# Kernel optimization log

Hardware: AMD Instinct MI355X
Metric: run time of the kernel (lower is better)

## Reference

```python
import jax, jax.numpy as jnp
import numpy as np

N_RAYS = 262144
N_COARSE = 64
N_SAMPLES = 256
TFINAL = 1e10  # sentinel far plane for last integration delta
EPS = 1e-5


def setup_inputs() -> dict:
    key = jax.random.key(0)
    k1, k2, k3, k4, k5 = jax.random.split(key, 5)
    tnear = jax.random.uniform(k1, (N_RAYS, 1), jnp.float32) * 0.5 + 0.1
    tfar = tnear + 1.0 + jax.random.uniform(k2, (N_RAYS, 1), jnp.float32) * 3.0
    dnorm = jax.random.uniform(k3, (N_RAYS, 1), jnp.float32) * 0.5 + 0.75
    # density at the coarse sample points (stands in for vol.sample(rays(ts_coarse)))
    density = jax.random.uniform(k4, (N_COARSE, N_RAYS, 1), jnp.float32) * 5.0
    # uniform draws for inverse-CDF sampling (torch.rand in the original)
    u = jax.random.uniform(k5, (N_RAYS, N_SAMPLES), jnp.float32)
    return {"tnear": tnear, "tfar": tfar, "dnorm": dnorm, "density": density, "u": u}


def _informed_sampler(tnear, tfar, dnorm, density, u):
    Tc = density.shape[0]
    # --- batch_linspace: coarse ts, shape (Tc, N, 1), timestep dim leading ---
    frac = (jnp.arange(Tc, dtype=tnear.dtype) / (Tc - 1)).reshape(Tc, 1, 1)
    ts = tnear[None] + (tfar - tnear)[None] * frac
    # --- integrate_timesteps: volume-rendering weights, shape (Tc, N, 1) ---
    delta = jnp.concatenate(
        [ts[1:] - ts[:-1], jnp.full_like(ts[:1], TFINAL) - ts[-1:]], axis=0
    )
    sd = density * delta * dnorm[None]            # sigma * dt * |d|
    sd_shift = jnp.concatenate([jnp.zeros_like(sd[:1]), sd[:-1]], axis=0)
    transmittance = jnp.exp(-jnp.cumsum(sd_shift, axis=0))
    weights = transmittance * (1.0 - jnp.exp(-sd))
    # --- sample_ray_step_informed: CDF build + inverse-CDF resampling ---
    w = jnp.moveaxis(weights[..., 0], 0, -1) + EPS          # (N, Tc)
    pdf = w / jnp.sum(w, axis=-1, keepdims=True)
    cdf = jnp.concatenate(
        [jnp.zeros_like(pdf[..., :1]), jnp.cumsum(pdf, axis=-1)], axis=-1
    )                                                        # (N, Tc+1)
    tsn = jnp.moveaxis(ts[..., 0], 0, -1)                    # (N, Tc)
    # bin edges: [tnear, midpoints, tfar] -> (N, Tc+1), Tc bins match Tc weights
    edges = jnp.concatenate(
        [tnear, 0.5 * (tsn[..., 1:] + tsn[..., :-1]), tfar], axis=-1
    )
    # per-ray searchsorted (vmap avoids a (N, S, Tc+1) dense compare)
    idx = jax.vmap(lambda c, q: jnp.searchsorted(c, q, side="right"))(cdf, u)
    idx = jnp.clip(idx, 1, Tc)
    below = idx - 1
    cdf_b = jnp.take_along_axis(cdf, below, axis=-1)
    cdf_a = jnp.take_along_axis(cdf, idx, axis=-1)
    e_b = jnp.take_along_axis(edges, below, axis=-1)
    e_a = jnp.take_along_axis(edges, idx, axis=-1)
    denom = cdf_a - cdf_b
    denom = jnp.where(denom < EPS, jnp.ones_like(denom), denom)
    t = (u - cdf_b) / denom
    samples = jnp.sort(e_b + t * (e_a - e_b), axis=-1)       # (N, n_samples)
    return jnp.moveaxis(samples, -1, 0)[..., None]           # (n_samples, N, 1)


def reference(tnear, tfar, dnorm, density, u):
    return _informed_sampler(tnear, tfar, dnorm, density, u)
```

## Files before the change

kernel.cpp:

```cpp
#include <hip/hip_runtime.h>
#include <stdint.h>

#define NRAYS   262144
#define NSAMP   256
#define RPB     16
#define TFINALF 1e10f
#define EPSF    1e-5f
#define CSTR    72
#define SSTR2   164
#define SKEW    20

template<int CTRL>
__device__ __forceinline__ uint32_t dppi(uint32_t x) {
    return (uint32_t)__builtin_amdgcn_update_dpp(0, (int)x, CTRL, 0xF, 0xF, false);
}
template<int CTRL>
__device__ __forceinline__ float dppf(float x) {
    return __int_as_float(__builtin_amdgcn_update_dpp(0, __float_as_int(x), CTRL, 0xF, 0xF, false));
}
template<int PAT>
__device__ __forceinline__ float swzf(float x) {
    return __int_as_float(__builtin_amdgcn_ds_swizzle(__float_as_int(x), PAT));
}

__device__ __forceinline__ float row16_iscan(float x) {
    x += dppf<0x111>(x);
    x += dppf<0x112>(x);
    x += dppf<0x114>(x);
    x += dppf<0x118>(x);
    return x;
}

__device__ __forceinline__ void celo(uint32_t& a, uint32_t& b) {
    uint32_t mn = min(a, b), mx = max(a, b);
    a = mn; b = mx;
}

template<int CTRL>
__device__ __forceinline__ void flipx(uint32_t w[16], bool up) {
#pragma unroll
    for (int p = 0; p < 8; ++p) {
        uint32_t a = w[p], b = w[15 - p];
        uint32_t oa = dppi<CTRL>(b);
        uint32_t ob = dppi<CTRL>(a);
        w[p]      = up ? max(a, oa) : min(a, oa);
        w[15 - p] = up ? max(b, ob) : min(b, ob);
    }
}

template<int CTRL>
__device__ __forceinline__ void jsx(uint32_t w[16], bool up) {
#pragma unroll
    for (int j = 0; j < 16; ++j) {
        uint32_t o = dppi<CTRL>(w[j]);
        w[j] = up ? max(w[j], o) : min(w[j], o);
    }
}
__device__ __forceinline__ void jsx_swz4(uint32_t w[16], bool up) {
#pragma unroll
    for (int j = 0; j < 16; ++j) {
        uint32_t o = (uint32_t)__builtin_amdgcn_ds_swizzle((int)w[j], 0x101F);
        w[j] = up ? max(w[j], o) : min(w[j], o);
    }
}

__device__ __forceinline__ void il_js8(uint32_t w[16]) {
#pragma unroll
    for (int j = 0; j < 8; ++j) celo(w[j], w[j + 8]);
}
__device__ __forceinline__ void il_js4(uint32_t w[16]) {
#pragma unroll
    for (int h = 0; h < 16; h += 8)
#pragma unroll
        for (int j = 0; j < 4; ++j) celo(w[h + j], w[h + j + 4]);
}
__device__ __forceinline__ void il_js2(uint32_t w[16]) {
#pragma unroll
    for (int h = 0; h < 16; h += 4) { celo(w[h], w[h + 2]); celo(w[h + 1], w[h + 3]); }
}
__device__ __forceinline__ void il_js1(uint32_t w[16]) {
#pragma unroll
    for (int j = 0; j < 16; j += 2) celo(w[j], w[j + 1]);
}

__device__ __forceinline__ void sort256(uint32_t w[16], int lane) {
    il_js1(w);
#pragma unroll
    for (int h = 0; h < 16; h += 4) { celo(w[h], w[h + 3]); celo(w[h + 1], w[h + 2]); }
    il_js1(w);
#pragma unroll
    for (int h = 0; h < 16; h += 8) {
        celo(w[h], w[h + 7]); celo(w[h + 1], w[h + 6]);
        celo(w[h + 2], w[h + 5]); celo(w[h + 3], w[h + 4]);
    }
    il_js2(w); il_js1(w);
#pragma unroll
    for (int j = 0; j < 8; ++j) celo(w[j], w[15 - j]);
    il_js4(w); il_js2(w); il_js1(w);

    const bool b1 = (lane & 1) != 0, b2 = (lane & 2) != 0;
    const bool b4 = (lane & 4) != 0, b8 = (lane & 8) != 0;
    flipx<0xB1>(w, b1);
    il_js8(w); il_js4(w); il_js2(w); il_js1(w);
    flipx<0x1B>(w, b2);
    jsx<0xB1>(w, b1);
    il_js8(w); il_js4(w); il_js2(w); il_js1(w);
    flipx<0x141>(w, b4);
    jsx<0x4E>(w, b2);
    jsx<0xB1>(w, b1);
    il_js8(w); il_js4(w); il_js2(w); il_js1(w);
    flipx<0x140>(w, b8);
    jsx_swz4(w, b4);
    jsx<0x4E>(w, b2);
    jsx<0xB1>(w, b1);
    il_js8(w); il_js4(w); il_js2(w); il_js1(w);
}

__global__ __launch_bounds__(256) void informed_sampler_kernel(
    const float* __restrict__ tnear,
    const float* __restrict__ tfar,
    const float* __restrict__ dnorm,
    const float* __restrict__ density,
    const float* __restrict__ u,
    float* __restrict__ out)
{
    __shared__ float s_cdf[8 + RPB * CSTR];
    __shared__ float s2[RPB * SSTR2];

    const int tid  = threadIdx.x;
    const int lane = tid & 63;
    const int lp   = lane & 15;
    const int c    = tid >> 4;
    const int r0   = blockIdx.x * RPB;
    const int r    = r0 + c;

    const float tn  = tnear[r];
    const float tff = tfar[r];
    const float dn  = dnorm[r];
    const float td  = tff - tn;
    const float inv63 = 1.0f / 63.0f;
    const float tdi = td * inv63;

    const float4* ub = reinterpret_cast<const float4*>(u + (size_t)r * NSAMP);
    uint32_t w[16];
    {
        float4 a0 = ub[lp * 4 + 0], a1 = ub[lp * 4 + 1], a2 = ub[lp * 4 + 2], a3 = ub[lp * 4 + 3];
        w[ 0]=__float_as_uint(a0.x); w[ 1]=__float_as_uint(a0.y); w[ 2]=__float_as_uint(a0.z); w[ 3]=__float_as_uint(a0.w);
        w[ 4]=__float_as_uint(a1.x); w[ 5]=__float_as_uint(a1.y); w[ 6]=__float_as_uint(a1.z); w[ 7]=__float_as_uint(a1.w);
        w[ 8]=__float_as_uint(a2.x); w[ 9]=__float_as_uint(a2.y); w[10]=__float_as_uint(a2.z); w[11]=__float_as_uint(a2.w);
        w[12]=__float_as_uint(a3.x); w[13]=__float_as_uint(a3.y); w[14]=__float_as_uint(a3.z); w[15]=__float_as_uint(a3.w);
    }

    const int b0 = lp * 4;
    float de0 = density[(size_t)(b0 + 0) * NRAYS + r];
    float de1 = density[(size_t)(b0 + 1) * NRAYS + r];
    float de2 = density[(size_t)(b0 + 2) * NRAYS + r];
    float de3 = density[(size_t)(b0 + 3) * NRAYS + r];

    float dl3 = (lp == 15) ? (TFINALF - (tn + td)) : tdi;
    float sd0 = de0 * tdi * dn, sd1 = de1 * tdi * dn, sd2 = de2 * tdi * dn, sd3 = de3 * dl3 * dn;

    float p0 = sd0, p1 = p0 + sd1, p2 = p1 + sd2, p3 = p2 + sd3;
    float tsc   = row16_iscan(p3);
    float carry = dppf<0x111>(tsc);
    float x0 = carry, x1 = carry + p0, x2 = carry + p1, x3 = carry + p2, x4 = carry + p3;
    float e0 = __expf(-x0), e1 = __expf(-x1), e2 = __expf(-x2), e3 = __expf(-x3), e4 = __expf(-x4);
    float wv0 = e0 - e1 + EPSF, wv1 = e1 - e2 + EPSF, wv2 = e2 - e3 + EPSF, wv3 = e3 - e4 + EPSF;
    float q0 = wv0, q1 = q0 + wv1, q2 = q1 + wv2, q3 = q2 + wv3;
    float tww = row16_iscan(q3);
    float cw  = dppf<0x111>(tww);
    float tot = swzf<0x1F0>(tww);
    float inv = __builtin_amdgcn_rcpf(tot);

    float rv0 = (cw + q0) * inv, rv1 = (cw + q1) * inv,
          rv2 = (cw + q2) * inv, rv3 = (cw + q3) * inv;
    float* cdfrow = &s_cdf[8 + c * CSTR];
    *reinterpret_cast<float4*>(cdfrow + b0) = make_float4(rv0, rv1, rv2, rv3);

    float r7  = swzf<0x030>(rv3);
    float r15 = swzf<0x070>(rv3);
    float r23 = swzf<0x0B0>(rv3);
    float r31 = swzf<0x0F0>(rv3);
    float r39 = swzf<0x130>(rv3);
    float r47 = swzf<0x170>(rv3);
    float r55 = swzf<0x1B0>(rv3);

    sort256(w, lane);

    __asm__ volatile("s_waitcnt lgkmcnt(0)" ::: "memory");

#pragma unroll
    for (int j = 0; j < 16; ++j) {
        float uq = __uint_as_float(w[j]);
        bool  c32 = (r31 <= uq);
        int   b   = c32 ? 32 : 0;
        float p16 = c32 ? r47 : r15;
        bool  t16 = (p16 <= uq);
        b += t16 ? 16 : 0;
        float pA = c32 ? r39 : r7;
        float pB = c32 ? r55 : r23;
        float p8 = t16 ? pB : pA;
        b += (p8 <= uq) ? 8 : 0;
        if (cdfrow[b + 3] <= uq) b += 4;
        if (cdfrow[b + 1] <= uq) b += 2;
        if (cdfrow[b]     <= uq) b += 1;
        float cbm = cdfrow[b - 1];
        float ca  = cdfrow[b];
        float cb  = (b == 0) ? 0.0f : cbm;
        float dnm = ca - cb;
        dnm = (dnm < EPSF) ? 1.0f : dnm;
        float fb = (float)b;
        float eb = fmaf(fmaxf(fb - 0.5f, 0.0f), tdi, tn);
        float ea = fmaf(fminf(fb + 0.5f, 63.0f), tdi, tn);
        float smp = eb + (uq - cb) * __builtin_amdgcn_rcpf(dnm) * (ea - eb);
        smp = fminf(fmaxf(smp, tn), tff);
        w[j] = __float_as_uint(smp);
    }

    float* s2row = &s2[c * SSTR2];
    const int g16 = tid >> 4;
    const int cc  = tid & 15;

    if (lp < 8) {
#pragma unroll
        for (int q = 0; q < 4; ++q)
            *reinterpret_cast<uint4*>(&s2row[lp * SKEW + q * 4]) =
                make_uint4(w[4 * q], w[4 * q + 1], w[4 * q + 2], w[4 * q + 3]);
    }
    __syncthreads();
#pragma unroll
    for (int it = 0; it < 8; ++it) {
        int s = it * 16 + g16;
        out[(size_t)s * NRAYS + r0 + cc] = s2[cc * SSTR2 + it * SKEW + g16];
    }
    __syncthreads();
    if (lp >= 8) {
#pragma unroll
        for (int q = 0; q < 4; ++q)
            *reinterpret_cast<uint4*>(&s2row[(lp - 8) * SKEW + q * 4]) =
                make_uint4(w[4 * q], w[4 * q + 1], w[4 * q + 2], w[4 * q + 3]);
    }
    __syncthreads();
#pragma unroll
    for (int it = 0; it < 8; ++it) {
        int s = 128 + it * 16 + g16;
        out[(size_t)s * NRAYS + r0 + cc] = s2[cc * SSTR2 + it * SKEW + g16];
    }
}

extern "C" void kernel_launch(void* const* d_in, const int* in_sizes, int n_in,
                              void* d_out, int out_size, void* d_ws, size_t ws_size,
                              hipStream_t stream) {
    const float* tnear   = (const float*)d_in[0];
    const float* tfar    = (const float*)d_in[1];
    const float* dnorm   = (const float*)d_in[2];
    const float* density = (const float*)d_in[3];
    const float* u       = (const float*)d_in[4];
    float* out = (float*)d_out;

    dim3 grid(NRAYS / RPB);
    dim3 block(256);
    hipLaunchKernelGGL(informed_sampler_kernel, grid, block, 0, stream,
                       tnear, tfar, dnorm, density, u, out);
}
```

Measured before the change: 197.8 us.

## Use med3 compare-exchange in sort and bpermute-based CDF search instead of LDS

The bitonic sort now works on float registers and picks the direction with v_med3 against a per-lane +/-inf selector, replacing the two-op max/min plus select. The per-ray CDF table in shared memory is removed. The last binary-search levels read CDF values from neighbouring lanes' registers through ds_bpermute, and the bracketing cdf values are carried through the search instead of being reloaded. This cuts VALU instructions in the sort and drops the shared-memory CDF store and scattered loads, at the cost of four bpermutes per sample.

```diff
diff --git a/kernel.cpp b/kernel.cpp
--- a/kernel.cpp
+++ b/kernel.cpp
@@ -6,14 +6,9 @@
 #define RPB     16
 #define TFINALF 1e10f
 #define EPSF    1e-5f
-#define CSTR    72
 #define SSTR2   164
 #define SKEW    20
 
-template<int CTRL>
-__device__ __forceinline__ uint32_t dppi(uint32_t x) {
-    return (uint32_t)__builtin_amdgcn_update_dpp(0, (int)x, CTRL, 0xF, 0xF, false);
-}
 template<int CTRL>
 __device__ __forceinline__ float dppf(float x) {
     return __int_as_float(__builtin_amdgcn_update_dpp(0, __float_as_int(x), CTRL, 0xF, 0xF, false));
@@ -21,6 +16,12 @@
 template<int PAT>
 __device__ __forceinline__ float swzf(float x) {
     return __int_as_float(__builtin_amdgcn_ds_swizzle(__float_as_int(x), PAT));
+}
+__device__ __forceinline__ float bpermf(int addr_bytes, float x) {
+    return __int_as_float(__builtin_amdgcn_ds_bpermute(addr_bytes, __float_as_int(x)));
+}
+__device__ __forceinline__ float med3(float a, float b, float s) {
+    return __builtin_amdgcn_fmed3f(a, b, s);
 }
 
 __device__ __forceinline__ float row16_iscan(float x) {
@@ -31,59 +32,55 @@
     return x;
 }
 
-__device__ __forceinline__ void celo(uint32_t& a, uint32_t& b) {
-    uint32_t mn = min(a, b), mx = max(a, b);
+__device__ __forceinline__ void celo(float& a, float& b) {
+    float mn = fminf(a, b), mx = fmaxf(a, b);
     a = mn; b = mx;
 }
 
 template<int CTRL>
-__device__ __forceinline__ void flipx(uint32_t w[16], bool up) {
+__device__ __forceinline__ void flipx(float w[16], float sel) {
 #pragma unroll
     for (int p = 0; p < 8; ++p) {
-        uint32_t a = w[p], b = w[15 - p];
-        uint32_t oa = dppi<CTRL>(b);
-        uint32_t ob = dppi<CTRL>(a);
-        w[p]      = up ? max(a, oa) : min(a, oa);
-        w[15 - p] = up ? max(b, ob) : min(b, ob);
+        float a = w[p], b = w[15 - p];
+        float oa = dppf<CTRL>(b);
+        float ob = dppf<CTRL>(a);
+        w[p]      = med3(a, oa, sel);
+        w[15 - p] = med3(b, ob, sel);
     }
 }
 
 template<int CTRL>
-__device__ __forceinline__ void jsx(uint32_t w[16], bool up) {
-#pragma unroll
-    for (int j = 0; j < 16; ++j) {
-        uint32_t o = dppi<CTRL>(w[j]);
-        w[j] = up ? max(w[j], o) : min(w[j], o);
-    }
-}
-__device__ __forceinline__ void jsx_swz4(uint32_t w[16], bool up) {
-#pragma unroll
-    for (int j = 0; j < 16; ++j) {
-        uint32_t o = (uint32_t)__builtin_amdgcn_ds_swizzle((int)w[j], 0x101F);
-        w[j] = up ? max(w[j], o) : min(w[j], o);
-    }
-}
-
-__device__ __forceinline__ void il_js8(uint32_t w[16]) {
+__device__ __forceinline__ void jsx(float w[16], float sel) {
+#pragma unroll
+    for (int j = 0; j < 16; ++j)
+        w[j] = med3(w[j], dppf<CTRL>(w[j]), sel);
+}
+__device__ __forceinline__ void jsx_swz4(float w[16], float sel) {
+#pragma unroll
+    for (int j = 0; j < 16; ++j)
+        w[j] = med3(w[j], swzf<0x101F>(w[j]), sel);
+}
+
+__device__ __forceinline__ void il_js8(float w[16]) {
 #pragma unroll
     for (int j = 0; j < 8; ++j) celo(w[j], w[j + 8]);
 }
-__device__ __forceinline__ void il_js4(uint32_t w[16]) {
+__device__ __forceinline__ void il_js4(float w[16]) {
 #pragma unroll
     for (int h = 0; h < 16; h += 8)
 #pragma unroll
         for (int j = 0; j < 4; ++j) celo(w[h + j], w[h + j + 4]);
 }
-__device__ __forceinline__ void il_js2(uint32_t w[16]) {
+__device__ __forceinline__ void il_js2(float w[16]) {
 #pragma unroll
     for (int h = 0; h < 16; h += 4) { celo(w[h], w[h + 2]); celo(w[h + 1], w[h + 3]); }
 }
-__device__ __forceinline__ void il_js1(uint32_t w[16]) {
+__device__ __forceinline__ void il_js1(float w[16]) {
 #pragma unroll
     for (int j = 0; j < 16; j += 2) celo(w[j], w[j + 1]);
 }
 
-__device__ __forceinline__ void sort256(uint32_t w[16], int lane) {
+__device__ __forceinline__ void sort256(float w[16], float s1, float s2m, float s4m, float s8m) {
     il_js1(w);
 #pragma unroll
     for (int h = 0; h < 16; h += 4) { celo(w[h], w[h + 3]); celo(w[h + 1], w[h + 2]); }
@@ -97,22 +94,19 @@
 #pragma unroll
     for (int j = 0; j < 8; ++j) celo(w[j], w[15 - j]);
     il_js4(w); il_js2(w); il_js1(w);
-
-    const bool b1 = (lane & 1) != 0, b2 = (lane & 2) != 0;
-    const bool b4 = (lane & 4) != 0, b8 = (lane & 8) != 0;
-    flipx<0xB1>(w, b1);
-    il_js8(w); il_js4(w); il_js2(w); il_js1(w);
-    flipx<0x1B>(w, b2);
-    jsx<0xB1>(w, b1);
-    il_js8(w); il_js4(w); il_js2(w); il_js1(w);
-    flipx<0x141>(w, b4);
-    jsx<0x4E>(w, b2);
-    jsx<0xB1>(w, b1);
-    il_js8(w); il_js4(w); il_js2(w); il_js1(w);
-    flipx<0x140>(w, b8);
-    jsx_swz4(w, b4);
-    jsx<0x4E>(w, b2);
-    jsx<0xB1>(w, b1);
+    flipx<0xB1>(w, s1);
+    il_js8(w); il_js4(w); il_js2(w); il_js1(w);
+    flipx<0x1B>(w, s2m);
+    jsx<0xB1>(w, s1);
+    il_js8(w); il_js4(w); il_js2(w); il_js1(w);
+    flipx<0x141>(w, s4m);
+    jsx<0x4E>(w, s2m);
+    jsx<0xB1>(w, s1);
+    il_js8(w); il_js4(w); il_js2(w); il_js1(w);
+    flipx<0x140>(w, s8m);
+    jsx_swz4(w, s4m);
+    jsx<0x4E>(w, s2m);
+    jsx<0xB1>(w, s1);
     il_js8(w); il_js4(w); il_js2(w); il_js1(w);
 }
 
@@ -124,7 +118,6 @@
     const float* __restrict__ u,
     float* __restrict__ out)
 {
-    __shared__ float s_cdf[8 + RPB * CSTR];
     __shared__ float s2[RPB * SSTR2];
 
     const int tid  = threadIdx.x;
@@ -141,14 +134,21 @@
     const float inv63 = 1.0f / 63.0f;
     const float tdi = td * inv63;
 
+    const float INF = __builtin_inff();
+    const float s1  = (lane & 1) ? INF : -INF;
+    const float s2m = (lane & 2) ? INF : -INF;
+    const float s4m = (lane & 4) ? INF : -INF;
+    const float s8m = (lane & 8) ? INF : -INF;
+    const int base4 = (lane & 48) << 2;
+
     const float4* ub = reinterpret_cast<const float4*>(u + (size_t)r * NSAMP);
-    uint32_t w[16];
+    float w[16];
     {
         float4 a0 = ub[lp * 4 + 0], a1 = ub[lp * 4 + 1], a2 = ub[lp * 4 + 2], a3 = ub[lp * 4 + 3];
-        w[ 0]=__float_as_uint(a0.x); w[ 1]=__float_as_uint(a0.y); w[ 2]=__float_as_uint(a0.z); w[ 3]=__float_as_uint(a0.w);
-        w[ 4]=__float_as_uint(a1.x); w[ 5]=__float_as_uint(a1.y); w[ 6]=__float_as_uint(a1.z); w[ 7]=__float_as_uint(a1.w);
-        w[ 8]=__float_as_uint(a2.x); w[ 9]=__float_as_uint(a2.y); w[10]=__float_as_uint(a2.z); w[11]=__float_as_uint(a2.w);
-        w[12]=__float_as_uint(a3.x); w[13]=__float_as_uint(a3.y); w[14]=__float_as_uint(a3.z); w[15]=__float_as_uint(a3.w);
+        w[ 0]=a0.x; w[ 1]=a0.y; w[ 2]=a0.z; w[ 3]=a0.w;
+        w[ 4]=a1.x; w[ 5]=a1.y; w[ 6]=a1.z; w[ 7]=a1.w;
+        w[ 8]=a2.x; w[ 9]=a2.y; w[10]=a2.z; w[11]=a2.w;
+        w[12]=a3.x; w[13]=a3.y; w[14]=a3.z; w[15]=a3.w;
     }
 
     const int b0 = lp * 4;
@@ -174,8 +174,7 @@
 
     float rv0 = (cw + q0) * inv, rv1 = (cw + q1) * inv,
           rv2 = (cw + q2) * inv, rv3 = (cw + q3) * inv;
-    float* cdfrow = &s_cdf[8 + c * CSTR];
-    *reinterpret_cast<float4*>(cdfrow + b0) = make_float4(rv0, rv1, rv2, rv3);
+    float row63 = tot * inv;
 
     float r7  = swzf<0x030>(rv3);
     float r15 = swzf<0x070>(rv3);
@@ -185,36 +184,50 @@
     float r47 = swzf<0x170>(rv3);
     float r55 = swzf<0x1B0>(rv3);
 
-    sort256(w, lane);
-
-    __asm__ volatile("s_waitcnt lgkmcnt(0)" ::: "memory");
+    sort256(w, s1, s2m, s4m, s8m);
 
 #pragma unroll
     for (int j = 0; j < 16; ++j) {
-        float uq = __uint_as_float(w[j]);
-        bool  c32 = (r31 <= uq);
-        int   b   = c32 ? 32 : 0;
-        float p16 = c32 ? r47 : r15;
-        bool  t16 = (p16 <= uq);
-        b += t16 ? 16 : 0;
-        float pA = c32 ? r39 : r7;
-        float pB = c32 ? r55 : r23;
-        float p8 = t16 ? pB : pA;
-        b += (p8 <= uq) ? 8 : 0;
-        if (cdfrow[b + 3] <= uq) b += 4;
-        if (cdfrow[b + 1] <= uq) b += 2;
-        if (cdfrow[b]     <= uq) b += 1;
-        float cbm = cdfrow[b - 1];
-        float ca  = cdfrow[b];
-        float cb  = (b == 0) ? 0.0f : cbm;
+        float uq = w[j];
+        float cbc = 0.0f, cac = row63;
+        bool a32 = (r31 <= uq);
+        int  b   = a32 ? 32 : 0;
+        cbc = a32 ? r31 : cbc;
+        cac = a32 ? cac : r31;
+        float p16 = a32 ? r47 : r15;
+        bool a16 = (p16 <= uq);
+        b += a16 ? 16 : 0;
+        cbc = a16 ? p16 : cbc;
+        cac = a16 ? cac : p16;
+        float pL = a16 ? r23 : r7;
+        float pH = a16 ? r55 : r39;
+        float p8 = a32 ? pH : pL;
+        bool a8 = (p8 <= uq);
+        b += a8 ? 8 : 0;
+        cbc = a8 ? p8 : cbc;
+        cac = a8 ? cac : p8;
+        float p4 = bpermf(base4 + b, rv3);
+        bool a4 = (p4 <= uq);
+        b += a4 ? 4 : 0;
+        cbc = a4 ? p4 : cbc;
+        cac = a4 ? cac : p4;
+        int ad = base4 + b;
+        float v0 = bpermf(ad, rv0);
+        float v1 = bpermf(ad, rv1);
+        float v2 = bpermf(ad, rv2);
+        bool a2 = (v1 <= uq);
+        float pl = a2 ? v2 : v0;
+        bool a1 = (pl <= uq);
+        b += (a2 ? 2 : 0) + (a1 ? 1 : 0);
+        float cb = a2 ? (a1 ? v2 : v1) : (a1 ? v0 : cbc);
+        float ca = a2 ? (a1 ? cac : v2) : (a1 ? v1 : v0);
         float dnm = ca - cb;
         dnm = (dnm < EPSF) ? 1.0f : dnm;
         float fb = (float)b;
         float eb = fmaf(fmaxf(fb - 0.5f, 0.0f), tdi, tn);
         float ea = fmaf(fminf(fb + 0.5f, 63.0f), tdi, tn);
         float smp = eb + (uq - cb) * __builtin_amdgcn_rcpf(dnm) * (ea - eb);
-        smp = fminf(fmaxf(smp, tn), tff);
-        w[j] = __float_as_uint(smp);
+        w[j] = fminf(fmaxf(smp, tn), tff);
     }
 
     float* s2row = &s2[c * SSTR2];
@@ -224,8 +237,8 @@
     if (lp < 8) {
 #pragma unroll
         for (int q = 0; q < 4; ++q)
-            *reinterpret_cast<uint4*>(&s2row[lp * SKEW + q * 4]) =
-                make_uint4(w[4 * q], w[4 * q + 1], w[4 * q + 2], w[4 * q + 3]);
+            *reinterpret_cast<float4*>(&s2row[lp * SKEW + q * 4]) =
+                make_float4(w[4 * q], w[4 * q + 1], w[4 * q + 2], w[4 * q + 3]);
     }
     __syncthreads();
 #pragma unroll
@@ -237,8 +250,8 @@
     if (lp >= 8) {
 #pragma unroll
         for (int q = 0; q < 4; ++q)
-            *reinterpret_cast<uint4*>(&s2row[(lp - 8) * SKEW + q * 4]) =
-                make_uint4(w[4 * q], w[4 * q + 1], w[4 * q + 2], w[4 * q + 3]);
+            *reinterpret_cast<float4*>(&s2row[(lp - 8) * SKEW + q * 4]) =
+                make_float4(w[4 * q], w[4 * q + 1], w[4 * q + 2], w[4 * q + 3]);
     }
     __syncthreads();
 #pragma unroll
```

After: 248.2 us. +25.5%, slower.
